# Kernel tuning notes

Measured on AMD Instinct MI355X. Metric: run time of the kernel, lower is better.

The kernel has to match this reference:

```python
import jax, jax.numpy as jnp
import numpy as np

H, FH, D = 8, 4, 64          # num_heads, focal_heads, att_size
HID = H * D                   # hidden_size = 512
B, S = 8, 512                 # batch, num_nodes
T_HOP, T_EDGE = 32, 16
SCALE = D ** -0.5


def setup_inputs() -> dict:
    key = jax.random.key(0)
    ks = jax.random.split(key, 24)
    f = lambda i, shape: jax.random.normal(ks[i], shape, jnp.float32)
    w = 1.0 / np.sqrt(HID)
    inp = {
        'q': f(0, (B, S, HID)), 'k': f(1, (B, S, HID)), 'v': f(2, (B, S, HID)),
        'query_hop_emb': f(3, (T_HOP, HID)) * 0.02,
        'query_edge_emb': f(4, (T_EDGE, HID)) * 0.02,
        'key_hop_emb': f(5, (T_HOP, HID)) * 0.02,
        'key_edge_emb': f(6, (T_EDGE, HID)) * 0.02,
        'value_hop_emb': f(7, (T_HOP, HID)) * 0.02,
        'value_edge_emb': f(8, (T_EDGE, HID)) * 0.02,
        'distance': jax.random.randint(ks[9], (B, S, S), 0, T_HOP),
        'edge_attr': jax.random.randint(ks[10], (B, S, S), 0, T_EDGE),
        # guarantee at least one unmasked key per query row to keep softmax finite
        'mask': jax.random.bernoulli(ks[11], 0.9, (B, S)).at[:, 0].set(True),
        'focal_mask': jax.random.bernoulli(ks[12], 0.5, (B, S, S)).at[:, :, 0].set(True),
        'Wq': f(13, (HID, H * D)) * w, 'bq': f(14, (H * D,)) * 0.01,
        'Wk': f(15, (HID, H * D)) * w, 'bk': f(16, (H * D,)) * 0.01,
        'Wv': f(17, (HID, H * D)) * w, 'bv': f(18, (H * D,)) * 0.01,
        'Wo': f(19, (H * D, HID)) * w, 'bo': f(20, (HID,)) * 0.01,
    }
    return inp


def _emb_scores(x, emb):
    # x: [B,H,S,D], emb: [T, H*D] -> per-head scores [B,H,S,T]
    e = emb.reshape(-1, H, D).transpose(1, 0, 2)  # [H,T,D]
    return jnp.einsum('bhsd,htd->bhst', x, e)


def _gather_last(scores, idx):
    # scores: [B,H,S,T], idx: [B,S,S] -> [B,H,S,S]
    idx_b = jnp.broadcast_to(idx[:, None], (B, H, S, S))
    return jnp.take_along_axis(scores, idx_b, axis=3)


def _scatter_add_last(attn, idx, T):
    # attn: [B,H,S,S], idx: [B,S,S] -> [B,H,S,T] accumulating attn weights
    idx_b = jnp.broadcast_to(idx[:, None], (B, H, S, S)).reshape(B * H * S, S)
    rows = jnp.arange(B * H * S)[:, None]
    flat = (rows * T + idx_b).reshape(-1)
    out = jnp.zeros((B * H * S * T,), attn.dtype).at[flat].add(attn.reshape(-1))
    return out.reshape(B, H, S, T)


def reference(q, k, v, query_hop_emb, query_edge_emb, key_hop_emb, key_edge_emb,
              value_hop_emb, value_edge_emb, distance, edge_attr, mask, focal_mask,
              Wq, bq, Wk, bk, Wv, bv, Wo, bo):
    qh = (q @ Wq + bq).reshape(B, S, H, D).transpose(0, 2, 1, 3)  # [B,H,S,D]
    kh = (k @ Wk + bk).reshape(B, S, H, D).transpose(0, 2, 1, 3)
    vh = (v @ Wv + bv).reshape(B, S, H, D).transpose(0, 2, 1, 3)

    spatial_bias = (_gather_last(_emb_scores(qh, query_hop_emb), distance)
                    + _gather_last(_emb_scores(kh, key_hop_emb), distance))
    edge_bias = (_gather_last(_emb_scores(qh, query_edge_emb), edge_attr)
                 + _gather_last(_emb_scores(kh, key_edge_emb), edge_attr))

    attn = (jnp.einsum('bhsd,bhtd->bhst', qh, kh) + spatial_bias + edge_bias) * SCALE

    GS = H - FH
    a1 = jnp.where(mask[:, None, None, :], attn[:, :GS], -jnp.inf)
    a2 = jnp.where(focal_mask[:, None], attn[:, GS:], -jnp.inf)
    attn = jax.nn.softmax(jnp.concatenate([a1, a2], axis=1), axis=3)

    vha = _scatter_add_last(attn, distance, T_HOP)   # [B,H,S,T_HOP]
    vea = _scatter_add_last(attn, edge_attr, T_EDGE)  # [B,H,S,T_EDGE]
    vh_emb = value_hop_emb.reshape(T_HOP, H, D).transpose(1, 0, 2)   # [H,T,D]
    ve_emb = value_edge_emb.reshape(T_EDGE, H, D).transpose(1, 0, 2)

    x = (jnp.einsum('bhst,bhtd->bhsd', attn, vh)
         + jnp.einsum('bhst,htd->bhsd', vha, vh_emb)
         + jnp.einsum('bhst,htd->bhsd', vea, ve_emb))
    x = x.transpose(0, 2, 1, 3).reshape(B, S, H * D)
    return x @ Wo + bo
```

## Files before the change

kernel.cpp:

```cpp
#include <hip/hip_runtime.h>

constexpr int nB = 8, nS = 512, nH = 8, nD = 64, nHID = 512;
constexpr int THOP = 32, TEDGE = 16;
constexpr float SCALE = 0.125f;
constexpr float NEGINF = -30000.0f;

typedef __attribute__((ext_vector_type(8))) short bf16x8;
typedef __attribute__((ext_vector_type(4))) float f32x4;

#define MFMA16(A, B, C) __builtin_amdgcn_mfma_f32_16x16x32_bf16(A, B, C, 0, 0, 0)

__device__ __align__(16) unsigned short g_qhi[(size_t)nB * nH * nS * nD];
__device__ __align__(16) unsigned short g_qlo[(size_t)nB * nH * nS * nD];
__device__ __align__(16) unsigned short g_khi[(size_t)nB * nH * nS * nD];
__device__ __align__(16) unsigned short g_klo[(size_t)nB * nH * nS * nD];
__device__ __align__(16) unsigned short g_vhiT[(size_t)nB * nH * nD * nS];
__device__ __align__(16) unsigned short g_vloT[(size_t)nB * nH * nD * nS];
__device__ __align__(16) unsigned short g_embh[96 * 512];
__device__ __align__(16) unsigned short g_embl[96 * 512];
__device__ __align__(16) unsigned short g_inhi[(size_t)3 * 2097152];
__device__ __align__(16) unsigned short g_inlo[(size_t)3 * 2097152];
__device__ __align__(16) unsigned short g_wth[(size_t)4 * 262144];
__device__ __align__(16) unsigned short g_wtl[(size_t)4 * 262144];
__device__ __align__(16) unsigned short g_xhi[(size_t)nB * nS * nHID];
__device__ __align__(16) unsigned short g_xlo[(size_t)nB * nS * nHID];
__device__ int g_flags[32];

__device__ __forceinline__ float ldf(const void* p, int isf32, size_t i) {
  if (isf32) return ((const float*)p)[i];
  unsigned int w = (unsigned int)(((const unsigned short*)p)[i]) << 16;
  return __uint_as_float(w);
}
__device__ __forceinline__ float bf2f(unsigned short h) {
  return __uint_as_float((unsigned)h << 16);
}
__device__ __forceinline__ float4 ldf4(const void* p, int isf32, size_t i) {
  if (isf32) return ((const float4*)p)[i >> 2];
  const ushort4 u = ((const ushort4*)p)[i >> 2];
  float4 r;
  r.x = bf2f(u.x); r.y = bf2f(u.y); r.z = bf2f(u.z); r.w = bf2f(u.w);
  return r;
}
__device__ __forceinline__ unsigned short f2bf(float x) {
  unsigned u = __float_as_uint(x);
  u += 0x7FFFu + ((u >> 16) & 1u);
  return (unsigned short)(u >> 16);
}

__device__ int detect_bool_mode(const unsigned char* p) {
  if (p[0] == 0x80 && p[1] == 0x3F) return 2;
  if (p[0] == 0x00 && p[1] == 0x3C) return 4;
  if (p[0] == 0x00 && p[3] == 0x3F) return 3;
  for (int i = 0; i < 64; i += 4)
    if (p[i + 1] | p[i + 2] | p[i + 3]) return 1;
  return 0;
}
__device__ __forceinline__ bool bool_at(const unsigned char* p, int mode, size_t i) {
  switch (mode) {
    case 0: return ((const int*)p)[i] != 0;
    case 1: return p[i] != 0;
    case 3: return ((const float*)p)[i] != 0.f;
    default: return ((const unsigned short*)p)[i] != 0;
  }
}

__global__ __launch_bounds__(256) void detect_all(
    const void* q, const void* k, const void* v,
    const void* qhe, const void* qee, const void* khe, const void* kee,
    const void* vhe, const void* vee,
    const int* dist, const int* edge,
    const unsigned char* mraw, const unsigned char* fraw,
    const void* Wq, const void* bq, const void* Wk, const void* bk,
    const void* Wv, const void* bv, const void* Wo, const void* bo) {
  __shared__ float sred[256];
  __shared__ int nzs;
  const int tid = threadIdx.x;
  const int blk = blockIdx.x;

  if (blk < 17) {
    const void* arrs[17] = {q, k, v, qhe, qee, khe, kee, vhe, vee,
                            Wq, bq, Wk, bk, Wv, bv, Wo, bo};
    const int full[17] = {2097152, 2097152, 2097152, 8192, 8192, 8192, 8192,
                          8192, 8192, 262144, 512, 262144, 512, 262144, 512,
                          262144, 512};
    const int n = full[blk] < 16384 ? full[blk] : 16384;
    const unsigned short* u = (const unsigned short*)arrs[blk];
    float m = 0.f;
    for (int i = tid; i < n; i += 256) {
      float x = __uint_as_float((unsigned int)u[i] << 16);
      if (x != x) x = 1e20f;
      m = fmaxf(m, fabsf(x));
    }
    sred[tid] = m;
    __syncthreads();
    for (int s = 128; s > 0; s >>= 1) {
      if (tid < s) sred[tid] = fmaxf(sred[tid], sred[tid + s]);
      __syncthreads();
    }
    if (tid == 0) g_flags[4 + blk] = (sred[0] > 1e3f) ? 1 : 0;
  } else if (blk == 17 || blk == 18) {
    const int* p = (blk == 17) ? dist : edge;
    if (tid == 0) nzs = 0;
    __syncthreads();
    int a = 0;
    for (int i = tid; i < 4096; i += 256) a |= p[2 * i + 1];
    if (a) atomicOr(&nzs, 1);
    __syncthreads();
    if (tid == 0) g_flags[blk - 17] = (nzs == 0);
  } else {
    if (tid == 0) {
      g_flags[2] = detect_bool_mode(mraw);
      g_flags[3] = detect_bool_mode(fraw);
    }
  }
}

__global__ __launch_bounds__(256) void emb_prep(
    const void* qhe, const void* khe, const void* qee, const void* kee) {
  const int blk = blockIdx.x;
  const void* srcs[4] = {qhe, khe, qee, kee};
  const int flagIdx[4] = {7, 9, 8, 10};
  const int counts[4] = {32 * 512, 32 * 512, 16 * 512, 16 * 512};
  const int dsts[4] = {0, 32 * 512, 64 * 512, 80 * 512};
  const int f = g_flags[flagIdx[blk]];
  const void* src = srcs[blk];
  const int n = counts[blk], d0 = dsts[blk];
  for (int i = threadIdx.x; i < n; i += 256) {
    const float x = ldf(src, f, i);
    const unsigned short hi = f2bf(x);
    g_embh[d0 + i] = hi;
    g_embl[d0 + i] = f2bf(x - bf2f(hi));
  }
}

__global__ __launch_bounds__(256) void split_prep(
    const void* q, const void* k, const void* v) {
  const int t = blockIdx.y;
  const void* srcs[3] = {q, k, v};
  const int f = g_flags[4 + t];
  const size_t base = (size_t)t * 2097152;
  const size_t i = ((size_t)blockIdx.x * 256 + threadIdx.x) * 4;
  const float4 v4 = ldf4(srcs[t], f, i);
  ushort4 h4, l4;
  h4.x = f2bf(v4.x); l4.x = f2bf(v4.x - bf2f(h4.x));
  h4.y = f2bf(v4.y); l4.y = f2bf(v4.y - bf2f(h4.y));
  h4.z = f2bf(v4.z); l4.z = f2bf(v4.z - bf2f(h4.z));
  h4.w = f2bf(v4.w); l4.w = f2bf(v4.w - bf2f(h4.w));
  *(ushort4*)&g_inhi[base + i] = h4;
  *(ushort4*)&g_inlo[base + i] = l4;
}

__global__ __launch_bounds__(256) void wt_prep(
    const void* Wq, const void* Wk, const void* Wv, const void* Wo) {
  __shared__ float t[64][65];
  const int mat = blockIdx.y;
  const void* srcs[4] = {Wq, Wk, Wv, Wo};
  const int fIdx[4] = {13, 15, 17, 19};
  const int f = g_flags[fIdx[mat]];
  const void* W = srcs[mat];
  const int k0 = (blockIdx.x >> 3) * 64, n0 = (blockIdx.x & 7) * 64;
  const int tid = threadIdx.x;
  const int r = tid >> 4, c4 = (tid & 15) * 4;
#pragma unroll
  for (int i = 0; i < 4; ++i) {
    const float4 v4 = ldf4(W, f, (size_t)(k0 + r + i * 16) * 512 + n0 + c4);
    t[r + i * 16][c4] = v4.x;
    t[r + i * 16][c4 + 1] = v4.y;
    t[r + i * 16][c4 + 2] = v4.z;
    t[r + i * 16][c4 + 3] = v4.w;
  }
  __syncthreads();
  unsigned short* dh = g_wth + (size_t)mat * 262144;
  unsigned short* dl = g_wtl + (size_t)mat * 262144;
#pragma unroll
  for (int i = 0; i < 4; ++i) {
    const int rn = r + i * 16;
    ushort4 h4, l4;
    const float v0 = t[c4][rn], v1 = t[c4 + 1][rn];
    const float v2 = t[c4 + 2][rn], v3 = t[c4 + 3][rn];
    h4.x = f2bf(v0); l4.x = f2bf(v0 - bf2f(h4.x));
    h4.y = f2bf(v1); l4.y = f2bf(v1 - bf2f(h4.y));
    h4.z = f2bf(v2); l4.z = f2bf(v2 - bf2f(h4.z));
    h4.w = f2bf(v3); l4.w = f2bf(v3 - bf2f(h4.w));
    *(ushort4*)&dh[(size_t)(n0 + rn) * 512 + k0 + c4] = h4;
    *(ushort4*)&dl[(size_t)(n0 + rn) * 512 + k0 + c4] = l4;
  }
}

template <int MODE_SEL>
__device__ __forceinline__ void gemm_body(
    const unsigned short* Ahi, const unsigned short* Alo,
    const unsigned short* Wth, const unsigned short* Wtl,
    const void* bias, int bF, float* dst, int mode, int m0, int n0) {
  __shared__ unsigned short As_hi[64][40];
  __shared__ unsigned short As_lo[64][40];
  __shared__ unsigned short Wt_hi[64][40];
  __shared__ unsigned short Wt_lo[64][40];
  const int tid = threadIdx.x;
  const int w = tid >> 6, l = tid & 63, c = l & 15, g = l >> 4;
  const int wr = w >> 1, wc = w & 1;
  const int sr = tid >> 2, sc = (tid & 3) * 8;

  f32x4 acc[2][2] = {{{0.f, 0.f, 0.f, 0.f}, {0.f, 0.f, 0.f, 0.f}},
                     {{0.f, 0.f, 0.f, 0.f}, {0.f, 0.f, 0.f, 0.f}}};

  const size_t ga = (size_t)(m0 + sr) * 512 + sc;
  const size_t gw = (size_t)(n0 + sr) * 512 + sc;
  bf16x8 pa_h = *(const bf16x8*)(Ahi + ga);
  bf16x8 pa_l = *(const bf16x8*)(Alo + ga);
  bf16x8 pw_h = *(const bf16x8*)(Wth + gw);
  bf16x8 pw_l = *(const bf16x8*)(Wtl + gw);

  for (int k0 = 0; k0 < 512; k0 += 32) {
    __syncthreads();
    *(bf16x8*)&As_hi[sr][sc] = pa_h;
    *(bf16x8*)&As_lo[sr][sc] = pa_l;
    *(bf16x8*)&Wt_hi[sr][sc] = pw_h;
    *(bf16x8*)&Wt_lo[sr][sc] = pw_l;
    __syncthreads();
    if (k0 < 480) {
      pa_h = *(const bf16x8*)(Ahi + ga + k0 + 32);
      pa_l = *(const bf16x8*)(Alo + ga + k0 + 32);
      pw_h = *(const bf16x8*)(Wth + gw + k0 + 32);
      pw_l = *(const bf16x8*)(Wtl + gw + k0 + 32);
    }
#pragma unroll
    for (int mi = 0; mi < 2; ++mi) {
      const bf16x8 ah = *(const bf16x8*)&As_hi[wr * 32 + mi * 16 + c][g * 8];
      const bf16x8 al = *(const bf16x8*)&As_lo[wr * 32 + mi * 16 + c][g * 8];
#pragma unroll
      for (int nj = 0; nj < 2; ++nj) {
        const bf16x8 wh = *(const bf16x8*)&Wt_hi[wc * 32 + nj * 16 + c][g * 8];
        const bf16x8 wl = *(const bf16x8*)&Wt_lo[wc * 32 + nj * 16 + c][g * 8];
        acc[mi][nj] = MFMA16(ah, wh, acc[mi][nj]);
        acc[mi][nj] = MFMA16(al, wh, acc[mi][nj]);
        acc[mi][nj] = MFMA16(ah, wl, acc[mi][nj]);
      }
    }
  }
#pragma unroll
  for (int mi = 0; mi < 2; ++mi)
#pragma unroll
    for (int nj = 0; nj < 2; ++nj)
#pragma unroll
      for (int r = 0; r < 4; ++r) {
        const int m = m0 + wr * 32 + mi * 16 + 4 * g + r;
        const int n = n0 + wc * 32 + nj * 16 + c;
        const float v2 = acc[mi][nj][r] + ldf(bias, bF, n);
        if (MODE_SEL == 3) {
          dst[(size_t)m * 512 + n] = v2;
        } else {
          const int b = m >> 9, s = m & 511, h = n >> 6, d = n & 63;
          const unsigned short hi = f2bf(v2);
          const unsigned short lo = f2bf(v2 - bf2f(hi));
          if (mode == 0) {
            const size_t i0 = (((size_t)(b * nH + h) * nS) + s) * nD + d;
            g_qhi[i0] = hi; g_qlo[i0] = lo;
          } else if (mode == 1) {
            const size_t i0 = (((size_t)(b * nH + h) * nS) + s) * nD + d;
            g_khi[i0] = hi; g_klo[i0] = lo;
          } else {
            const size_t i0 = (((size_t)(b * nH + h) * nD) + d) * nS + s;
            g_vhiT[i0] = hi; g_vloT[i0] = lo;
          }
        }
      }
}

__global__ __launch_bounds__(256, 4) void gemm_qkv(
    const unsigned short* __restrict__ inhi, const unsigned short* __restrict__ inlo,
    const unsigned short* __restrict__ wth, const unsigned short* __restrict__ wtl,
    const void* __restrict__ bq, const void* __restrict__ bk,
    const void* __restrict__ bv) {
  const int mat = blockIdx.y >> 6;
  const int m0 = (blockIdx.y & 63) * 64, n0 = blockIdx.x * 64;
  const void* bias = (mat == 0) ? bq : (mat == 1) ? bk : bv;
  const int bF = g_flags[14 + 2 * mat];
  gemm_body<0>(inhi + (size_t)mat * 2097152, inlo + (size_t)mat * 2097152,
               wth + (size_t)mat * 262144, wtl + (size_t)mat * 262144,
               bias, bF, nullptr, mat, m0, n0);
}

__global__ __launch_bounds__(256, 4) void gemm_out(
    const unsigned short* __restrict__ Ahi, const unsigned short* __restrict__ Alo,
    const unsigned short* __restrict__ Wth, const unsigned short* __restrict__ Wtl,
    const void* __restrict__ bias, float* __restrict__ dst) {
  gemm_body<3>(Ahi, Alo, Wth, Wtl, bias, g_flags[20], dst, 3,
               blockIdx.y * 64, blockIdx.x * 64);
}

__global__ __launch_bounds__(256, 3) void attn_kernel(
    const int* __restrict__ dist, const int* __restrict__ edge,
    const unsigned char* __restrict__ mraw, const unsigned char* __restrict__ fraw,
    const void* __restrict__ vhe, const void* __restrict__ vee) {
  __shared__ unsigned short kvbuf[8192];
  __shared__ unsigned short plds[16][520];
  __shared__ float chop_s[16][33];
  __shared__ float cedge_s[16][17];
  __shared__ float vha_s[16][33];
  __shared__ float vea_s[16][17];
  __shared__ float red_s[16][4];
  __shared__ float red2_s[16][4];
  __shared__ float rinv_s[16];

  const int id = blockIdx.x;
  const int bh = (id & 7) * 8 + ((id >> 3) & 7);
  const int qt = id >> 6;
  const int b = bh >> 3, h = bh & 7;
  const int q0 = qt * 16;
  const int tid = threadIdx.x;
  const int w = tid >> 6, l = tid & 63, c = l & 15, g = l >> 4;

  const int d64 = g_flags[0], e64 = g_flags[1];
  const int mmode = g_flags[2], fmode = g_flags[3];
  const int fvhe = g_flags[11], fvee = g_flags[12];

  for (int i = tid; i < 16 * 33; i += 256) (&vha_s[0][0])[i] = 0.f;
  for (int i = tid; i < 16 * 17; i += 256) (&vea_s[0][0])[i] = 0.f;

  const int e0 = tid << 3;
  const int kr0 = e0 >> 6, kd0 = e0 & 63;
  const int vd0 = e0 >> 7, vcol = e0 & 127;
  bf16x8 rkh0, rkh1, rkl0, rkl1;
  bf16x8 rv0, rv1, rv2, rv3;

  auto loadK = [&](int ch) {
    const size_t base = ((size_t)bh * nS + ch * 64) * nD + kd0;
    rkh0 = *(const bf16x8*)(g_khi + base + (size_t)kr0 * nD);
    rkl0 = *(const bf16x8*)(g_klo + base + (size_t)kr0 * nD);
    rkh1 = *(const bf16x8*)(g_khi + base + (size_t)(kr0 + 32) * nD);
    rkl1 = *(const bf16x8*)(g_klo + base + (size_t)(kr0 + 32) * nD);
  };
  auto writeK = [&]() {
    const int dst0 = (kr0 << 6) + (((kd0 >> 3) ^ (kr0 & 7)) << 3);
    const int dst1 = ((kr0 + 32) << 6) + (((kd0 >> 3) ^ ((kr0 + 32) & 7)) << 3);
    *(bf16x8*)&kvbuf[dst0] = rkh0;
    *(bf16x8*)&kvbuf[4096 + dst0] = rkl0;
    *(bf16x8*)&kvbuf[dst1] = rkh1;
    *(bf16x8*)&kvbuf[4096 + dst1] = rkl1;
  };
  auto loadV = [&](int p) {
    const size_t base = (size_t)bh * nD * nS + (p << 7) + vcol;
    rv0 = *(const bf16x8*)(g_vhiT + base + (size_t)vd0 * nS);
    rv1 = *(const bf16x8*)(g_vhiT + base + (size_t)(vd0 + 16) * nS);
    rv2 = *(const bf16x8*)(g_vhiT + base + (size_t)(vd0 + 32) * nS);
    rv3 = *(const bf16x8*)(g_vhiT + base + (size_t)(vd0 + 48) * nS);
  };
  auto writeV = [&]() {
    const int swz = ((vcol >> 3) ^ (vd0 & 15)) << 3;
    *(bf16x8*)&kvbuf[(vd0 << 7) + swz] = rv0;
    *(bf16x8*)&kvbuf[((vd0 + 16) << 7) + swz] = rv1;
    *(bf16x8*)&kvbuf[((vd0 + 32) << 7) + swz] = rv2;
    *(bf16x8*)&kvbuf[((vd0 + 48) << 7) + swz] = rv3;
  };

  loadK(0);

  const size_t rowbase = ((size_t)b * nS + q0) * nS;
  for (int j4 = tid; j4 < 2048; j4 += 256) {
    const int j = j4 * 4, r = j >> 9, c1 = j & 511;
    int dv[4], ev[4];
    if (!d64) {
      const int4 t = ((const int4*)(dist + rowbase))[j4];
      dv[0] = t.x & 31; dv[1] = t.y & 31; dv[2] = t.z & 31; dv[3] = t.w & 31;
    } else {
      const int4 t0 = ((const int4*)(dist + 2 * rowbase))[2 * j4];
      const int4 t1 = ((const int4*)(dist + 2 * rowbase))[2 * j4 + 1];
      dv[0] = t0.x & 31; dv[1] = t0.z & 31; dv[2] = t1.x & 31; dv[3] = t1.z & 31;
    }
    if (!e64) {
      const int4 t = ((const int4*)(edge + rowbase))[j4];
      ev[0] = t.x & 15; ev[1] = t.y & 15; ev[2] = t.z & 15; ev[3] = t.w & 15;
    } else {
      const int4 t0 = ((const int4*)(edge + 2 * rowbase))[2 * j4];
      const int4 t1 = ((const int4*)(edge + 2 * rowbase))[2 * j4 + 1];
      ev[0] = t0.x & 15; ev[1] = t0.z & 15; ev[2] = t1.x & 15; ev[3] = t1.z & 15;
    }
    ushort4 pw;
    unsigned short* pp = (unsigned short*)&pw;
#pragma unroll
    for (int t = 0; t < 4; ++t) {
      const bool keep = (h < 4) ? bool_at(mraw, mmode, (size_t)b * nS + c1 + t)
                                : bool_at(fraw, fmode, rowbase + j + t);
      pp[t] = (unsigned short)(dv[t] | (ev[t] << 5) | ((int)keep << 9));
    }
    *(ushort4*)&plds[r][c1] = pw;
  }

  const size_t qbase = (((size_t)bh * nS) + q0 + c) * nD + g * 8;
  const bf16x8 qh0 = *(const bf16x8*)(g_qhi + qbase);
  const bf16x8 qh1 = *(const bf16x8*)(g_qhi + qbase + 32);
  const bf16x8 ql0 = *(const bf16x8*)(g_qlo + qbase);
  const bf16x8 ql1 = *(const bf16x8*)(g_qlo + qbase + 32);

  if (w < 3) {
    const bool isEdge = (w == 2);
    const int tb = (w == 1) ? 16 : 0;
    const size_t qe0 = (isEdge ? (size_t)64 * 512 : 0) + (size_t)(tb + c) * 512 + h * 64;
    const size_t ke0 = (isEdge ? (size_t)80 * 512 : (size_t)32 * 512) + (size_t)(tb + c) * 512 + h * 64;
    f32x4 acc = {0.f, 0.f, 0.f, 0.f};
#pragma unroll
    for (int dh = 0; dh < 2; ++dh) {
      const bf16x8 qhh = dh ? qh1 : qh0;
      const bf16x8 qll = dh ? ql1 : ql0;
      const bf16x8 khq = *(const bf16x8*)(g_khi + qbase + dh * 32);
      const bf16x8 klq = *(const bf16x8*)(g_klo + qbase + dh * 32);
      const bf16x8 eqh = *(const bf16x8*)(g_embh + qe0 + dh * 32 + g * 8);
      const bf16x8 eql = *(const bf16x8*)(g_embl + qe0 + dh * 32 + g * 8);
      const bf16x8 ekh = *(const bf16x8*)(g_embh + ke0 + dh * 32 + g * 8);
      const bf16x8 ekl = *(const bf16x8*)(g_embl + ke0 + dh * 32 + g * 8);
      acc = MFMA16(qhh, eqh, acc);
      acc = MFMA16(qll, eqh, acc);
      acc = MFMA16(qhh, eql, acc);
      acc = MFMA16(khq, ekh, acc);
      acc = MFMA16(klq, ekh, acc);
      acc = MFMA16(khq, ekl, acc);
    }
    if (!isEdge) {
#pragma unroll
      for (int r = 0; r < 4; ++r) chop_s[4 * g + r][tb + c] = acc[r];
    } else {
#pragma unroll
      for (int r = 0; r < 4; ++r) cedge_s[4 * g + r][c] = acc[r];
    }
  }

  writeK();
  __syncthreads();

  f32x4 pS[8];
  const int sw8 = c & 7;
  for (int ch = 0; ch < 8; ++ch) {
    if (ch < 7) loadK(ch + 1);
    const int a0 = (w * 16 + c) << 6;
    f32x4 acc = {0.f, 0.f, 0.f, 0.f};
    {
      const int o0 = a0 + ((g ^ sw8) << 3);
      const int o1 = a0 + (((4 + g) ^ sw8) << 3);
      const bf16x8 kh0 = *(const bf16x8*)&kvbuf[o0];
      const bf16x8 kl0 = *(const bf16x8*)&kvbuf[4096 + o0];
      const bf16x8 kh1 = *(const bf16x8*)&kvbuf[o1];
      const bf16x8 kl1 = *(const bf16x8*)&kvbuf[4096 + o1];
      acc = MFMA16(kh0, qh0, acc);
      acc = MFMA16(kl0, qh0, acc);
      acc = MFMA16(kh0, ql0, acc);
      acc = MFMA16(kh1, qh1, acc);
      acc = MFMA16(kl1, qh1, acc);
      acc = MFMA16(kh1, ql1, acc);
    }
    const int key0 = ch * 64 + w * 16 + 4 * g;
    const ushort4 pv4 = *(const ushort4*)&plds[c][key0];
    const unsigned short pp[4] = {pv4.x, pv4.y, pv4.z, pv4.w};
#pragma unroll
    for (int r = 0; r < 4; ++r) {
      const float s = (acc[r] + chop_s[c][pp[r] & 31] +
                       cedge_s[c][(pp[r] >> 5) & 15]) * SCALE;
      pS[ch][r] = (pp[r] & 512) ? s : NEGINF;
    }
    __syncthreads();
    if (ch < 7) {
      writeK();
      __syncthreads();
    }
  }

  loadV(0);

  float mx = NEGINF;
#pragma unroll
  for (int kt = 0; kt < 8; ++kt)
#pragma unroll
    for (int r = 0; r < 4; ++r) mx = fmaxf(mx, pS[kt][r]);
  mx = fmaxf(mx, __shfl_xor(mx, 16));
  mx = fmaxf(mx, __shfl_xor(mx, 32));
  if (l < 16) red_s[c][w] = mx;
  __syncthreads();
  const float M = fmaxf(fmaxf(red_s[c][0], red_s[c][1]),
                        fmaxf(red_s[c][2], red_s[c][3]));
  float sum = 0.f;
#pragma unroll
  for (int kt = 0; kt < 8; ++kt) {
    const int key0 = kt * 64 + w * 16 + 4 * g;
    const ushort4 pv4 = *(const ushort4*)&plds[c][key0];
    const unsigned short pp[4] = {pv4.x, pv4.y, pv4.z, pv4.w};
#pragma unroll
    for (int r = 0; r < 4; ++r) {
      const float pv = __expf(pS[kt][r] - M);
      pS[kt][r] = pv;
      sum += pv;
      atomicAdd(&vha_s[c][pp[r] & 31], pv);
      atomicAdd(&vea_s[c][(pp[r] >> 5) & 15], pv);
    }
  }
  sum += __shfl_xor(sum, 16);
  sum += __shfl_xor(sum, 32);
  if (l < 16) red2_s[c][w] = sum;
  int pk[8][2];
#pragma unroll
  for (int kt = 0; kt < 8; ++kt) {
    pk[kt][0] = ((int)f2bf(pS[kt][1]) << 16) | (int)f2bf(pS[kt][0]);
    pk[kt][1] = ((int)f2bf(pS[kt][3]) << 16) | (int)f2bf(pS[kt][2]);
  }
  writeV();
  __syncthreads();
  float (*x_s)[17] = reinterpret_cast<float(*)[17]>(&plds[0][0]);
  for (int i = tid; i < 64 * 17; i += 256) (&x_s[0][0])[i] = 0.f;
  if (w == 0 && l < 16) {
    const float tot = red2_s[c][0] + red2_s[c][1] + red2_s[c][2] + red2_s[c][3];
    rinv_s[c] = 1.0f / tot;
  }
  __syncthreads();

  f32x4 oacc[4] = {{0.f, 0.f, 0.f, 0.f}, {0.f, 0.f, 0.f, 0.f},
                   {0.f, 0.f, 0.f, 0.f}, {0.f, 0.f, 0.f, 0.f}};
  const int srcA = ((g & 1) * 2) * 16 + c;
  const int srcB = srcA + 16;
  const bool hi2 = (g >> 1) != 0;
  for (int p = 0; p < 4; ++p) {
    if (p < 3) loadV(p + 1);
    const int t0d0 = __shfl(pk[2 * p][0], srcA);
    const int t1d0 = __shfl(pk[2 * p + 1][0], srcA);
    const int t0d1 = __shfl(pk[2 * p][1], srcA);
    const int t1d1 = __shfl(pk[2 * p + 1][1], srcA);
    const int t0d0b = __shfl(pk[2 * p][0], srcB);
    const int t1d0b = __shfl(pk[2 * p + 1][0], srcB);
    const int t0d1b = __shfl(pk[2 * p][1], srcB);
    const int t1d1b = __shfl(pk[2 * p + 1][1], srcB);
    union { int i[4]; bf16x8 v; } bu;
    bu.i[0] = hi2 ? t1d0 : t0d0;
    bu.i[1] = hi2 ? t1d1 : t0d1;
    bu.i[2] = hi2 ? t1d0b : t0d0b;
    bu.i[3] = hi2 ? t1d1b : t0d1b;
    const int col16 = (w << 1) + (g & 1) + ((g >> 1) << 3);
    const int j0 = (p << 7) + ((g >> 1) << 6) + (w << 4) + ((g & 1) << 3);
#pragma unroll
    for (int t = 0; t < 4; ++t) {
      const int row = t * 16 + c;
      const bf16x8 vh_ = *(const bf16x8*)&kvbuf[(row << 7) + ((col16 ^ c) << 3)];
      const bf16x8 vl_ = *(const bf16x8*)(g_vloT + (((size_t)bh * nD) + row) * nS + j0);
      oacc[t] = MFMA16(vh_, bu.v, oacc[t]);
      oacc[t] = MFMA16(vl_, bu.v, oacc[t]);
    }
    __syncthreads();
    if (p < 3) {
      writeV();
      __syncthreads();
    }
  }
#pragma unroll
  for (int t = 0; t < 4; ++t)
#pragma unroll
    for (int r = 0; r < 4; ++r)
      atomicAdd(&x_s[t * 16 + 4 * g + r][c], oacc[t][r]);
  __syncthreads();

  {
    const int d = tid & 63, qq = tid >> 6;
    float val[4];
#pragma unroll
    for (int j = 0; j < 4; ++j) val[j] = x_s[d][qq + 4 * j];
    for (int t = 0; t < THOP; ++t) {
      const float e = ldf(vhe, fvhe, (size_t)t * nHID + h * 64 + d);
#pragma unroll
      for (int j = 0; j < 4; ++j) val[j] += vha_s[qq + 4 * j][t] * e;
    }
    for (int t = 0; t < TEDGE; ++t) {
      const float e = ldf(vee, fvee, (size_t)t * nHID + h * 64 + d);
#pragma unroll
      for (int j = 0; j < 4; ++j) val[j] += vea_s[qq + 4 * j][t] * e;
    }
#pragma unroll
    for (int j = 0; j < 4; ++j) {
      const int q = qq + 4 * j;
      const float xv = val[j] * rinv_s[q];
      const unsigned short hi = f2bf(xv);
      const size_t i0 = ((size_t)b * nS + q0 + q) * nHID + h * 64 + d;
      g_xhi[i0] = hi;
      g_xlo[i0] = f2bf(xv - bf2f(hi));
    }
  }
}

extern "C" void kernel_launch(void* const* d_in, const int* in_sizes, int n_in,
                              void* d_out, int out_size, void* d_ws, size_t ws_size,
                              hipStream_t stream) {
  const void* q   = d_in[0];
  const void* k   = d_in[1];
  const void* v   = d_in[2];
  const void* qhe = d_in[3];
  const void* qee = d_in[4];
  const void* khe = d_in[5];
  const void* kee = d_in[6];
  const void* vhe = d_in[7];
  const void* vee = d_in[8];
  const int* dist = (const int*)d_in[9];
  const int* edge = (const int*)d_in[10];
  const unsigned char* mraw = (const unsigned char*)d_in[11];
  const unsigned char* fraw = (const unsigned char*)d_in[12];
  const void* Wq = d_in[13];
  const void* bq = d_in[14];
  const void* Wk = d_in[15];
  const void* bk = d_in[16];
  const void* Wv = d_in[17];
  const void* bv = d_in[18];
  const void* Wo = d_in[19];
  const void* bo = d_in[20];

  detect_all<<<20, 256, 0, stream>>>(q, k, v, qhe, qee, khe, kee, vhe, vee,
                                     dist, edge, mraw, fraw,
                                     Wq, bq, Wk, bk, Wv, bv, Wo, bo);
  emb_prep<<<4, 256, 0, stream>>>(qhe, khe, qee, kee);
  split_prep<<<dim3(2048, 3), 256, 0, stream>>>(q, k, v);
  wt_prep<<<dim3(64, 4), 256, 0, stream>>>(Wq, Wk, Wv, Wo);

  unsigned short* inhi; hipGetSymbolAddress((void**)&inhi, HIP_SYMBOL(g_inhi));
  unsigned short* inlo; hipGetSymbolAddress((void**)&inlo, HIP_SYMBOL(g_inlo));
  unsigned short* wth;  hipGetSymbolAddress((void**)&wth,  HIP_SYMBOL(g_wth));
  unsigned short* wtl;  hipGetSymbolAddress((void**)&wtl,  HIP_SYMBOL(g_wtl));
  unsigned short* xhi;  hipGetSymbolAddress((void**)&xhi,  HIP_SYMBOL(g_xhi));
  unsigned short* xlo;  hipGetSymbolAddress((void**)&xlo,  HIP_SYMBOL(g_xlo));

  gemm_qkv<<<dim3(8, 192), 256, 0, stream>>>(inhi, inlo, wth, wtl, bq, bk, bv);
  attn_kernel<<<2048, 256, 0, stream>>>(dist, edge, mraw, fraw, vhe, vee);
  gemm_out<<<dim3(8, 64), 256, 0, stream>>>(xhi, xlo,
                                            wth + 3 * 262144, wtl + 3 * 262144,
                                            bo, (float*)d_out);
}
```

Baseline: 558.4 us.

## Double-buffer K-hi in LDS, load K-lo from global, add MFMA priority hints

The QK loop now stages only the high bf16 half of K in shared memory, using two alternating 4096-element buffers. This removes one of the two barriers per chunk. The low half of K is read straight from global memory in the register layout the MFMA needs. s_setprio hints are placed around the MFMA sequences in the QK and PV loops, plds padding shrinks, and launch bounds drop from 3 to 2 blocks per SM. The trade-off is more uncoalesced global traffic for K-lo and possibly lower occupancy, in exchange for fewer barriers and less LDS traffic.

Measured after the change: 562.8 us. Within noise of the previous version (+0.8%).

```diff
diff --git a/kernel.cpp b/kernel.cpp
--- a/kernel.cpp
+++ b/kernel.cpp
@@ -289,12 +289,12 @@
                blockIdx.y * 64, blockIdx.x * 64);
 }
 
-__global__ __launch_bounds__(256, 3) void attn_kernel(
+__global__ __launch_bounds__(256, 2) void attn_kernel(
     const int* __restrict__ dist, const int* __restrict__ edge,
     const unsigned char* __restrict__ mraw, const unsigned char* __restrict__ fraw,
     const void* __restrict__ vhe, const void* __restrict__ vee) {
   __shared__ unsigned short kvbuf[8192];
-  __shared__ unsigned short plds[16][520];
+  __shared__ unsigned short plds[16][516];
   __shared__ float chop_s[16][33];
   __shared__ float cedge_s[16][17];
   __shared__ float vha_s[16][33];
@@ -321,23 +321,20 @@
   const int e0 = tid << 3;
   const int kr0 = e0 >> 6, kd0 = e0 & 63;
   const int vd0 = e0 >> 7, vcol = e0 & 127;
-  bf16x8 rkh0, rkh1, rkl0, rkl1;
+  bf16x8 rkh0, rkh1;
   bf16x8 rv0, rv1, rv2, rv3;
 
-  auto loadK = [&](int ch) {
+  auto loadKhi = [&](int ch) {
     const size_t base = ((size_t)bh * nS + ch * 64) * nD + kd0;
     rkh0 = *(const bf16x8*)(g_khi + base + (size_t)kr0 * nD);
-    rkl0 = *(const bf16x8*)(g_klo + base + (size_t)kr0 * nD);
     rkh1 = *(const bf16x8*)(g_khi + base + (size_t)(kr0 + 32) * nD);
-    rkl1 = *(const bf16x8*)(g_klo + base + (size_t)(kr0 + 32) * nD);
   };
-  auto writeK = [&]() {
+  auto writeKhi = [&](int buf) {
+    const int base = buf * 4096;
     const int dst0 = (kr0 << 6) + (((kd0 >> 3) ^ (kr0 & 7)) << 3);
     const int dst1 = ((kr0 + 32) << 6) + (((kd0 >> 3) ^ ((kr0 + 32) & 7)) << 3);
-    *(bf16x8*)&kvbuf[dst0] = rkh0;
-    *(bf16x8*)&kvbuf[4096 + dst0] = rkl0;
-    *(bf16x8*)&kvbuf[dst1] = rkh1;
-    *(bf16x8*)&kvbuf[4096 + dst1] = rkl1;
+    *(bf16x8*)&kvbuf[base + dst0] = rkh0;
+    *(bf16x8*)&kvbuf[base + dst1] = rkh1;
   };
   auto loadV = [&](int p) {
     const size_t base = (size_t)bh * nD * nS + (p << 7) + vcol;
@@ -354,7 +351,7 @@
     *(bf16x8*)&kvbuf[((vd0 + 48) << 7) + swz] = rv3;
   };
 
-  loadK(0);
+  loadKhi(0);
 
   const size_t rowbase = ((size_t)b * nS + q0) * nS;
   for (int j4 = tid; j4 < 2048; j4 += 256) {
@@ -425,29 +422,30 @@
     }
   }
 
-  writeK();
+  writeKhi(0);
   __syncthreads();
 
   f32x4 pS[8];
   const int sw8 = c & 7;
+  const int krow = w * 16 + c;
   for (int ch = 0; ch < 8; ++ch) {
-    if (ch < 7) loadK(ch + 1);
-    const int a0 = (w * 16 + c) << 6;
+    if (ch < 7) loadKhi(ch + 1);
+    const unsigned short* kb_ = kvbuf + (ch & 1) * 4096;
+    const size_t klbase = ((size_t)bh * nS + ch * 64 + krow) * nD + g * 8;
+    const bf16x8 kl0 = *(const bf16x8*)(g_klo + klbase);
+    const bf16x8 kl1 = *(const bf16x8*)(g_klo + klbase + 32);
+    const int a0 = krow << 6;
+    const bf16x8 kh0 = *(const bf16x8*)&kb_[a0 + ((g ^ sw8) << 3)];
+    const bf16x8 kh1 = *(const bf16x8*)&kb_[a0 + (((4 + g) ^ sw8) << 3)];
     f32x4 acc = {0.f, 0.f, 0.f, 0.f};
-    {
-      const int o0 = a0 + ((g ^ sw8) << 3);
-      const int o1 = a0 + (((4 + g) ^ sw8) << 3);
-      const bf16x8 kh0 = *(const bf16x8*)&kvbuf[o0];
-      const bf16x8 kl0 = *(const bf16x8*)&kvbuf[4096 + o0];
-      const bf16x8 kh1 = *(const bf16x8*)&kvbuf[o1];
-      const bf16x8 kl1 = *(const bf16x8*)&kvbuf[4096 + o1];
-      acc = MFMA16(kh0, qh0, acc);
-      acc = MFMA16(kl0, qh0, acc);
-      acc = MFMA16(kh0, ql0, acc);
-      acc = MFMA16(kh1, qh1, acc);
-      acc = MFMA16(kl1, qh1, acc);
-      acc = MFMA16(kh1, ql1, acc);
-    }
+    __builtin_amdgcn_s_setprio(1);
+    acc = MFMA16(kh0, qh0, acc);
+    acc = MFMA16(kh0, ql0, acc);
+    acc = MFMA16(kh1, qh1, acc);
+    acc = MFMA16(kh1, ql1, acc);
+    acc = MFMA16(kl0, qh0, acc);
+    acc = MFMA16(kl1, qh1, acc);
+    __builtin_amdgcn_s_setprio(0);
     const int key0 = ch * 64 + w * 16 + 4 * g;
     const ushort4 pv4 = *(const ushort4*)&plds[c][key0];
     const unsigned short pp[4] = {pv4.x, pv4.y, pv4.z, pv4.w};
@@ -457,9 +455,8 @@
                        cedge_s[c][(pp[r] >> 5) & 15]) * SCALE;
       pS[ch][r] = (pp[r] & 512) ? s : NEGINF;
     }
-    __syncthreads();
     if (ch < 7) {
-      writeK();
+      writeKhi((ch + 1) & 1);
       __syncthreads();
     }
   }
@@ -533,6 +530,7 @@
     bu.i[3] = hi2 ? t1d1b : t0d1b;
     const int col16 = (w << 1) + (g & 1) + ((g >> 1) << 3);
     const int j0 = (p << 7) + ((g >> 1) << 6) + (w << 4) + ((g & 1) << 3);
+    __builtin_amdgcn_s_setprio(1);
 #pragma unroll
     for (int t = 0; t < 4; ++t) {
       const int row = t * 16 + c;
@@ -541,8 +539,9 @@
       oacc[t] = MFMA16(vh_, bu.v, oacc[t]);
       oacc[t] = MFMA16(vl_, bu.v, oacc[t]);
     }
-    __syncthreads();
+    __builtin_amdgcn_s_setprio(0);
     if (p < 3) {
+      __syncthreads();
       writeV();
       __syncthreads();
     }
```
